# Kernel optimization log

Hardware: AMD Instinct MI355X
Metric: run time of the kernel (lower is better)

The kernel has to match this reference:

```python
import jax, jax.numpy as jnp
import numpy as np

N_NODES = 100000
N_EDGES = 3200000
IN_CH = 128
HID = 64
OUT_CH = 40


def setup_inputs() -> dict:
    key = jax.random.key(0)
    ks = jax.random.split(key, 12)
    x = jax.random.normal(ks[0], (N_NODES, IN_CH), dtype=jnp.float32)
    edge_index = jax.random.randint(ks[1], (2, N_EDGES), 0, N_NODES, dtype=jnp.int64)
    def lin(k, fan_in, fan_out):
        bound = 1.0 / np.sqrt(fan_in)
        kw, kb = jax.random.split(k)
        W = jax.random.uniform(kw, (fan_in, fan_out), minval=-bound, maxval=bound, dtype=jnp.float32)
        b = jax.random.uniform(kb, (fan_out,), minval=-bound, maxval=bound, dtype=jnp.float32)
        return W, b
    W1, b1 = lin(ks[2], IN_CH, HID)   # nn1 layer 1
    W2, b2 = lin(ks[3], HID, HID)     # nn1 layer 2
    W3, b3 = lin(ks[4], HID, HID)     # nn2 layer 1
    W4, b4 = lin(ks[5], HID, HID)     # nn2 layer 2
    Wf, bf = lin(ks[6], HID, OUT_CH)  # final fc
    return {"x": x, "edge_index": edge_index,
            "W1": W1, "b1": b1, "W2": W2, "b2": b2,
            "W3": W3, "b3": b3, "W4": W4, "b4": b4,
            "Wf": Wf, "bf": bf}


def _gin_conv(x, src, dst, W_a, b_a, W_b, b_b):
    # GINConv (eps=0): out = MLP(x + sum_{j->i} x_j)
    agg = jax.ops.segment_sum(x[src], dst, num_segments=x.shape[0])
    h = x + agg
    h = jax.nn.relu(h @ W_a + b_a)
    return h @ W_b + b_b


def reference(x, edge_index, W1, b1, W2, b2, W3, b3, W4, b4, Wf, bf):
    src, dst = edge_index[0], edge_index[1]
    h = _gin_conv(x, src, dst, W1, b1, W2, b2)
    h = jax.nn.relu(h)  # dropout is identity at eval
    h = _gin_conv(h, src, dst, W3, b3, W4, b4)
    h = jax.nn.relu(h)
    logits = h @ Wf + bf
    return jax.nn.log_softmax(logits, axis=1)
```

## Files before the change

kernel.cpp:

```cpp
#include <hip/hip_runtime.h>
#include <math.h>

#define N_NODES_C 100000
#define N_EDGES_C 3200000
#define NB 782
#define BNODES 128
#define LDS_CAP 6144
#define CHUNK 8192
#define NBLK 391

typedef unsigned short u16;
typedef __attribute__((ext_vector_type(8))) short short8v;
typedef __attribute__((ext_vector_type(4))) float float4v;

__device__ __forceinline__ float bf2f(u16 u) {
    unsigned int t = ((unsigned int)u) << 16;
    return __uint_as_float(t);
}
__device__ __forceinline__ u16 f2bf(float f) {
    unsigned int x = __float_as_uint(f);
    x += 0x7fffu + ((x >> 16) & 1u);
    return (u16)(x >> 16);
}


__global__ __launch_bounds__(256) void passA_hist_kernel(const int* __restrict__ dst,
                                                         int* __restrict__ cnt, int n_edges) {
    __shared__ int h[NB];
    for (int i = threadIdx.x; i < NB; i += 256) h[i] = 0;
    __syncthreads();
    const int blk = blockIdx.x;
    const int e0 = blk * CHUNK;
    const int cntE = min(CHUNK, n_edges - e0);
    for (int i = threadIdx.x * 4; i < cntE; i += 1024) {
        int4 d4 = *(const int4*)&dst[e0 + i];
        atomicAdd(&h[d4.x >> 7], 1); atomicAdd(&h[d4.y >> 7], 1);
        atomicAdd(&h[d4.z >> 7], 1); atomicAdd(&h[d4.w >> 7], 1);
    }
    __syncthreads();
    for (int i = threadIdx.x; i < NB; i += 256) cnt[i * NBLK + blk] = h[i];
}

__global__ __launch_bounds__(256) void scan_chunks_kernel(int* __restrict__ a, int n, int* __restrict__ bsums) {
    __shared__ int s[256];
    const int tid = threadIdx.x;
    int base = blockIdx.x * 1024 + tid * 4;
    int v[4];
#pragma unroll
    for (int i = 0; i < 4; ++i) v[i] = (base + i < n) ? a[base + i] : 0;
    int tsum = v[0] + v[1] + v[2] + v[3];
    s[tid] = tsum;
    __syncthreads();
    for (int off = 1; off < 256; off <<= 1) {
        int t = (tid >= off) ? s[tid - off] : 0;
        __syncthreads();
        s[tid] += t;
        __syncthreads();
    }
    int run = s[tid] - tsum;
#pragma unroll
    for (int i = 0; i < 4; ++i) {
        run += v[i];
        if (base + i < n) a[base + i] = run;
    }
    if (tid == 255) bsums[blockIdx.x] = s[255];
}

__global__ __launch_bounds__(512) void scan_sums_kernel(int* __restrict__ bsums, int nb) {
    __shared__ int s[512];
    const int tid = threadIdx.x;
    int v = (tid < nb) ? bsums[tid] : 0;
    s[tid] = v;
    __syncthreads();
    for (int off = 1; off < 512; off <<= 1) {
        int t = (tid >= off) ? s[tid - off] : 0;
        __syncthreads();
        s[tid] += t;
        __syncthreads();
    }
    if (tid < nb) bsums[tid] = s[tid] - v;
}

__global__ __launch_bounds__(256) void scan_add_kernel(int* __restrict__ a, int n, const int* __restrict__ bsums) {
    int base = blockIdx.x * 1024 + threadIdx.x * 4;
    int add = bsums[blockIdx.x];
#pragma unroll
    for (int i = 0; i < 4; ++i)
        if (base + i < n) a[base + i] += add;
}

__global__ __launch_bounds__(1024) void boffs_kernel(const int* __restrict__ incl,
                                                     int* __restrict__ boffs,
                                                     int* __restrict__ offs) {
    const int b = threadIdx.x;
    if (b < NB) boffs[b] = b ? incl[b * NBLK - 1] : 0;
    if (b == 0) {
        int total = incl[NB * NBLK - 1];
        boffs[NB] = total;
        offs[N_NODES_C] = total;
    }
}

__global__ __launch_bounds__(256) void passB_sort_kernel(const int* __restrict__ src,
                                                         const int* __restrict__ dst,
                                                         const int* __restrict__ incl,
                                                         unsigned int* __restrict__ stage,
                                                         int n_edges) {
    __shared__ unsigned int spack[CHUNK];
    __shared__ int hist[NB];
    __shared__ int lcur[NB];
    __shared__ int tsum[256];
    const int blk = blockIdx.x, tid = threadIdx.x;
    const int e0 = blk * CHUNK;
    const int cntE = min(CHUNK, n_edges - e0);

    for (int b = tid; b < NB; b += 256) hist[b] = 0;
    __syncthreads();

    for (int i = tid * 4; i < cntE; i += 1024) {
        int4 d4 = *(const int4*)&dst[e0 + i];
        atomicAdd(&hist[d4.x >> 7], 1); atomicAdd(&hist[d4.y >> 7], 1);
        atomicAdd(&hist[d4.z >> 7], 1); atomicAdd(&hist[d4.w >> 7], 1);
    }
    __syncthreads();

    {
        int loc[4];
        const int bi = tid * 4;
        int s = 0;
#pragma unroll
        for (int k = 0; k < 4; ++k) {
            int idx = bi + k;
            loc[k] = (idx < NB) ? hist[idx] : 0;
            s += loc[k];
        }
        tsum[tid] = s;
        __syncthreads();
        for (int off = 1; off < 256; off <<= 1) {
            int t = (tid >= off) ? tsum[tid - off] : 0;
            __syncthreads();
            tsum[tid] += t;
            __syncthreads();
        }
        int run = tsum[tid] - s;
#pragma unroll
        for (int k = 0; k < 4; ++k) {
            int idx = bi + k;
            if (idx < NB) {
                int h = loc[k];
                hist[idx] = run;
                lcur[idx] = run;
                run += h;
            }
        }
    }
    __syncthreads();

    for (int i = tid * 4; i < cntE; i += 1024) {
        int4 d4 = *(const int4*)&dst[e0 + i];
        int4 s4 = *(const int4*)&src[e0 + i];
        int p;
        p = atomicAdd(&lcur[d4.x >> 7], 1); spack[p] = (unsigned)s4.x | (((unsigned)d4.x & 127u) << 17);
        p = atomicAdd(&lcur[d4.y >> 7], 1); spack[p] = (unsigned)s4.y | (((unsigned)d4.y & 127u) << 17);
        p = atomicAdd(&lcur[d4.z >> 7], 1); spack[p] = (unsigned)s4.z | (((unsigned)d4.z & 127u) << 17);
        p = atomicAdd(&lcur[d4.w >> 7], 1); spack[p] = (unsigned)s4.w | (((unsigned)d4.w & 127u) << 17);
    }
    __syncthreads();

    for (int b = tid; b < NB; b += 256) {
        int l0 = hist[b];
        int l1 = (b + 1 < NB) ? hist[b + 1] : cntE;
        int idx = b * NBLK + blk;
        int g0 = idx ? incl[idx - 1] : 0;
        for (int j = l0; j < l1; ++j) stage[g0 + (j - l0)] = spack[j];
    }
}

__global__ __launch_bounds__(256) void bucket_finalize_kernel(const unsigned int* __restrict__ stage,
                                                              const int* __restrict__ boffs,
                                                              int* __restrict__ offs,
                                                              int* __restrict__ srcs) {
    __shared__ int hist[BNODES];
    __shared__ int excl[BNODES];
    __shared__ int curs[BNODES];
    __shared__ int sbuf[LDS_CAP];
    const int b = blockIdx.x, tid = threadIdx.x;
    const int base = boffs[b];
    const int count = boffs[b + 1] - base;
    const int n0 = b * BNODES;
    for (int i = tid; i < BNODES; i += 256) hist[i] = 0;
    __syncthreads();
    for (int i = tid; i < count; i += 256) {
        unsigned int w = stage[base + i];
        atomicAdd(&hist[w >> 17], 1);
    }
    __syncthreads();
    if (tid < BNODES) excl[tid] = hist[tid];
    __syncthreads();
    for (int off = 1; off < BNODES; off <<= 1) {
        int t = 0;
        if (tid < BNODES && tid >= off) t = excl[tid - off];
        __syncthreads();
        if (tid < BNODES) excl[tid] += t;
        __syncthreads();
    }
    if (tid < BNODES) {
        int ex = excl[tid] - hist[tid];
        int n = n0 + tid;
        if (n < N_NODES_C) offs[n] = base + ex;
        curs[tid] = ex;
    }
    __syncthreads();
    if (count <= LDS_CAP) {
        for (int i = tid; i < count; i += 256) {
            unsigned int w = stage[base + i];
            int p = atomicAdd(&curs[w >> 17], 1);
            sbuf[p] = (int)(w & 0x1FFFFu);
        }
        __syncthreads();
        for (int i = tid; i < count; i += 256) srcs[base + i] = sbuf[i];
    } else {
        for (int i = tid; i < count; i += 256) {
            unsigned int w = stage[base + i];
            int p = atomicAdd(&curs[w >> 17], 1);
            srcs[base + p] = (int)(w & 0x1FFFFu);
        }
    }
}


__global__ __launch_bounds__(256) void gather64v_kernel(const u16* __restrict__ feat,
                                                        const int* __restrict__ offs,
                                                        const int* __restrict__ srcs,
                                                        const float* __restrict__ bias,
                                                        u16* __restrict__ out, int n_nodes) {
    const int wave = threadIdx.x >> 6;
    const int lane = threadIdx.x & 63;
    const int grp  = lane >> 4;
    const int cl   = lane & 15;
    const int n = blockIdx.x * 4 + wave;
    if (n >= n_nodes) return;

    float a0 = 0.f, a1 = 0.f, a2 = 0.f, a3 = 0.f;
    if (grp == 0) {
        ushort4 v = *(const ushort4*)&feat[(size_t)n * 64 + cl * 4];
        a0 = bf2f(v.x); a1 = bf2f(v.y); a2 = bf2f(v.z); a3 = bf2f(v.w);
    }
    const int s0 = offs[n], s1 = offs[n + 1];
    int i = s0;
    for (; i + 32 <= s1; i += 32) {
        int r[8];
#pragma unroll
        for (int u = 0; u < 8; ++u) r[u] = srcs[i + u * 4 + grp];
        ushort4 v[8];
#pragma unroll
        for (int u = 0; u < 8; ++u) v[u] = *(const ushort4*)&feat[(size_t)r[u] * 64 + cl * 4];
#pragma unroll
        for (int u = 0; u < 8; ++u) {
            a0 += bf2f(v[u].x); a1 += bf2f(v[u].y); a2 += bf2f(v[u].z); a3 += bf2f(v[u].w);
        }
    }
    for (; i + 8 <= s1; i += 8) {
        int ra = srcs[i + grp];
        int rb = srcs[i + 4 + grp];
        ushort4 va = *(const ushort4*)&feat[(size_t)ra * 64 + cl * 4];
        ushort4 vb = *(const ushort4*)&feat[(size_t)rb * 64 + cl * 4];
        a0 += bf2f(va.x); a1 += bf2f(va.y); a2 += bf2f(va.z); a3 += bf2f(va.w);
        a0 += bf2f(vb.x); a1 += bf2f(vb.y); a2 += bf2f(vb.z); a3 += bf2f(vb.w);
    }
    for (; i + 4 <= s1; i += 4) {
        int rr = srcs[i + grp];
        ushort4 v = *(const ushort4*)&feat[(size_t)rr * 64 + cl * 4];
        a0 += bf2f(v.x); a1 += bf2f(v.y); a2 += bf2f(v.z); a3 += bf2f(v.w);
    }
    if (i + grp < s1) {
        int rr = srcs[i + grp];
        ushort4 v = *(const ushort4*)&feat[(size_t)rr * 64 + cl * 4];
        a0 += bf2f(v.x); a1 += bf2f(v.y); a2 += bf2f(v.z); a3 += bf2f(v.w);
    }
    a0 += __shfl_xor(a0, 16); a1 += __shfl_xor(a1, 16);
    a2 += __shfl_xor(a2, 16); a3 += __shfl_xor(a3, 16);
    a0 += __shfl_xor(a0, 32); a1 += __shfl_xor(a1, 32);
    a2 += __shfl_xor(a2, 32); a3 += __shfl_xor(a3, 32);
    if (lane < 16) {
        float4 b = *(const float4*)&bias[cl * 4];
        ushort4 o;
        o.x = f2bf(fmaxf(a0 + b.x, 0.f));
        o.y = f2bf(fmaxf(a1 + b.y, 0.f));
        o.z = f2bf(fmaxf(a2 + b.z, 0.f));
        o.w = f2bf(fmaxf(a3 + b.w, 0.f));
        *(ushort4*)&out[(size_t)n * 64 + cl * 4] = o;
    }
}

#define GIN_STEP(ai, i)                                                                               \
    acc[i][0] += ai.x * w0.x; acc[i][1] += ai.x * w0.y; acc[i][2] += ai.x * w0.z; acc[i][3] += ai.x * w0.w; \
    acc[i][0] += ai.y * w1.x; acc[i][1] += ai.y * w1.y; acc[i][2] += ai.y * w1.z; acc[i][3] += ai.y * w1.w; \
    acc[i][0] += ai.z * w2.x; acc[i][1] += ai.z * w2.y; acc[i][2] += ai.z * w2.z; acc[i][3] += ai.z * w2.w; \
    acc[i][0] += ai.w * w3.x; acc[i][1] += ai.w * w3.y; acc[i][2] += ai.w * w3.z; acc[i][3] += ai.w * w3.w;


__global__ __launch_bounds__(256) void dense128_kernel(const float* __restrict__ in,
                                                       const float* __restrict__ W,
                                                       u16* __restrict__ out, int n_nodes) {
    __shared__ float sW[128 * 64];
    const int tid = threadIdx.x;
    for (int i = tid; i < 128 * 16; i += 256) ((float4*)sW)[i] = ((const float4*)W)[i];
    __syncthreads();
    const int tj = tid & 15, tn = tid >> 4;
    const int j0 = tj * 4, n0 = blockIdx.x * 64 + tn * 4;
    const int r0 = min(n0 + 0, n_nodes - 1), r1 = min(n0 + 1, n_nodes - 1);
    const int r2 = min(n0 + 2, n_nodes - 1), r3 = min(n0 + 3, n_nodes - 1);
    float acc[4][4];
#pragma unroll
    for (int i = 0; i < 4; ++i)
#pragma unroll
        for (int j = 0; j < 4; ++j) acc[i][j] = 0.f;
#pragma unroll 4
    for (int k = 0; k < 128; k += 4) {
        float4 a0 = *(const float4*)&in[(size_t)r0 * 128 + k];
        float4 a1 = *(const float4*)&in[(size_t)r1 * 128 + k];
        float4 a2 = *(const float4*)&in[(size_t)r2 * 128 + k];
        float4 a3 = *(const float4*)&in[(size_t)r3 * 128 + k];
        float4 w0 = *(const float4*)&sW[(k + 0) * 64 + j0];
        float4 w1 = *(const float4*)&sW[(k + 1) * 64 + j0];
        float4 w2 = *(const float4*)&sW[(k + 2) * 64 + j0];
        float4 w3 = *(const float4*)&sW[(k + 3) * 64 + j0];
        GIN_STEP(a0, 0) GIN_STEP(a1, 1) GIN_STEP(a2, 2) GIN_STEP(a3, 3)
    }
#pragma unroll
    for (int i = 0; i < 4; ++i) {
        int n = n0 + i;
        if (n < n_nodes) {
            ushort4 o;
            o.x = f2bf(acc[i][0]); o.y = f2bf(acc[i][1]);
            o.z = f2bf(acc[i][2]); o.w = f2bf(acc[i][3]);
            *(ushort4*)&out[(size_t)n * 64 + j0] = o;
        }
    }
}


__global__ __launch_bounds__(256) void mfma_w2w3_kernel(const u16* __restrict__ in,
                                                        const float* __restrict__ W2,
                                                        const float* __restrict__ b2,
                                                        const float* __restrict__ W3,
                                                        u16* __restrict__ out, int n_nodes) {
    __shared__ u16 w2f[4096];
    __shared__ u16 w3f[4096];
    __shared__ u16 sT[64 * 72];
    const int tid = threadIdx.x;
    for (int idx = tid; idx < 4096; idx += 256) {
        int frag = idx >> 9;
        int within = idx & 511;
        int lane = within >> 3;
        int i = within & 7;
        int kt = frag >> 2, jt = frag & 3;
        int k = kt * 32 + (lane >> 4) * 8 + i;
        int j = jt * 16 + (lane & 15);
        w2f[idx] = f2bf(W2[k * 64 + j]);
        w3f[idx] = f2bf(W3[k * 64 + j]);
    }
    __syncthreads();
    const int w = tid >> 6, l = tid & 63;
    const int nbase = blockIdx.x * 64 + w * 16;
    const int arow = min(nbase + (l & 15), n_nodes - 1);
    short8v a0 = *(const short8v*)&in[(size_t)arow * 64 + (l >> 4) * 8];
    short8v a1 = *(const short8v*)&in[(size_t)arow * 64 + 32 + (l >> 4) * 8];
#pragma unroll
    for (int jt = 0; jt < 4; ++jt) {
        float bv = b2[jt * 16 + (l & 15)];
        float4v acc = {bv, bv, bv, bv};
        acc = __builtin_amdgcn_mfma_f32_16x16x32_bf16(a0, *(short8v*)&w2f[(0 * 4 + jt) * 512 + l * 8], acc, 0, 0, 0);
        acc = __builtin_amdgcn_mfma_f32_16x16x32_bf16(a1, *(short8v*)&w2f[(1 * 4 + jt) * 512 + l * 8], acc, 0, 0, 0);
#pragma unroll
        for (int r = 0; r < 4; ++r) {
            int row = w * 16 + (l >> 4) * 4 + r;
            sT[row * 72 + jt * 16 + (l & 15)] = f2bf(fmaxf(acc[r], 0.f));
        }
    }
    __syncthreads();
    const int trow = w * 16 + (l & 15);
    short8v t0 = *(short8v*)&sT[trow * 72 + (l >> 4) * 8];
    short8v t1 = *(short8v*)&sT[trow * 72 + 32 + (l >> 4) * 8];
#pragma unroll
    for (int jt = 0; jt < 4; ++jt) {
        float4v acc = {0.f, 0.f, 0.f, 0.f};
        acc = __builtin_amdgcn_mfma_f32_16x16x32_bf16(t0, *(short8v*)&w3f[(0 * 4 + jt) * 512 + l * 8], acc, 0, 0, 0);
        acc = __builtin_amdgcn_mfma_f32_16x16x32_bf16(t1, *(short8v*)&w3f[(1 * 4 + jt) * 512 + l * 8], acc, 0, 0, 0);
#pragma unroll
        for (int r = 0; r < 4; ++r) {
            int n = nbase + (l >> 4) * 4 + r;
            if (n < n_nodes) out[(size_t)n * 64 + jt * 16 + (l & 15)] = f2bf(acc[r]);
        }
    }
}


__global__ __launch_bounds__(256) void mfma_w4final_kernel(const u16* __restrict__ in,
                                                           const float* __restrict__ W4,
                                                           const float* __restrict__ b4,
                                                           const float* __restrict__ Wf,
                                                           const float* __restrict__ bfin,
                                                           float* __restrict__ out, int n_nodes) {
    __shared__ u16 w4f[4096];
    __shared__ u16 wff[3072];
    __shared__ u16 sT[64 * 72];
    __shared__ float sLog[64 * 40];
    const int tid = threadIdx.x;
    for (int idx = tid; idx < 4096; idx += 256) {
        int frag = idx >> 9;
        int within = idx & 511;
        int lane = within >> 3;
        int i = within & 7;
        int kt = frag >> 2, jt = frag & 3;
        int k = kt * 32 + (lane >> 4) * 8 + i;
        int j = jt * 16 + (lane & 15);
        w4f[idx] = f2bf(W4[k * 64 + j]);
    }
    for (int idx = tid; idx < 3072; idx += 256) {
        int frag = idx >> 9;
        int within = idx & 511;
        int lane = within >> 3;
        int i = within & 7;
        int kt = frag / 3, jt = frag % 3;
        int k = kt * 32 + (lane >> 4) * 8 + i;
        int j = jt * 16 + (lane & 15);
        wff[idx] = (j < 40) ? f2bf(Wf[k * 40 + j]) : (u16)0;
    }
    __syncthreads();
    const int w = tid >> 6, l = tid & 63;
    const int nbase = blockIdx.x * 64 + w * 16;
    const int arow = min(nbase + (l & 15), n_nodes - 1);
    short8v a0 = *(const short8v*)&in[(size_t)arow * 64 + (l >> 4) * 8];
    short8v a1 = *(const short8v*)&in[(size_t)arow * 64 + 32 + (l >> 4) * 8];
#pragma unroll
    for (int jt = 0; jt < 4; ++jt) {
        float bv = b4[jt * 16 + (l & 15)];
        float4v acc = {bv, bv, bv, bv};
        acc = __builtin_amdgcn_mfma_f32_16x16x32_bf16(a0, *(short8v*)&w4f[(0 * 4 + jt) * 512 + l * 8], acc, 0, 0, 0);
        acc = __builtin_amdgcn_mfma_f32_16x16x32_bf16(a1, *(short8v*)&w4f[(1 * 4 + jt) * 512 + l * 8], acc, 0, 0, 0);
#pragma unroll
        for (int r = 0; r < 4; ++r) {
            int row = w * 16 + (l >> 4) * 4 + r;
            sT[row * 72 + jt * 16 + (l & 15)] = f2bf(fmaxf(acc[r], 0.f));
        }
    }
    __syncthreads();
    const int trow = w * 16 + (l & 15);
    short8v t0 = *(short8v*)&sT[trow * 72 + (l >> 4) * 8];
    short8v t1 = *(short8v*)&sT[trow * 72 + 32 + (l >> 4) * 8];
#pragma unroll
    for (int jt = 0; jt < 3; ++jt) {
        int col = jt * 16 + (l & 15);
        float bv = (col < 40) ? bfin[col] : 0.f;
        float4v acc = {bv, bv, bv, bv};
        acc = __builtin_amdgcn_mfma_f32_16x16x32_bf16(t0, *(short8v*)&wff[(0 * 3 + jt) * 512 + l * 8], acc, 0, 0, 0);
        acc = __builtin_amdgcn_mfma_f32_16x16x32_bf16(t1, *(short8v*)&wff[(1 * 3 + jt) * 512 + l * 8], acc, 0, 0, 0);
#pragma unroll
        for (int r = 0; r < 4; ++r) {
            int row = w * 16 + (l >> 4) * 4 + r;
            if (col < 40) sLog[row * 40 + col] = acc[r];
        }
    }
    __syncthreads();
    if (tid < 64) {
        const int nl = tid;
        const int n = blockIdx.x * 64 + nl;
        if (n < n_nodes) {
            float m = -1e30f;
            for (int j = 0; j < 40; ++j) m = fmaxf(m, sLog[nl * 40 + j]);
            float s = 0.f;
            for (int j = 0; j < 40; ++j) s += expf(sLog[nl * 40 + j] - m);
            float lse = m + logf(s);
            for (int j = 0; j < 40; j += 4) {
                float4 o;
                o.x = sLog[nl * 40 + j + 0] - lse;
                o.y = sLog[nl * 40 + j + 1] - lse;
                o.z = sLog[nl * 40 + j + 2] - lse;
                o.w = sLog[nl * 40 + j + 3] - lse;
                *(float4*)&out[(size_t)n * 40 + j] = o;
            }
        }
    }
}


extern "C" void kernel_launch(void* const* d_in, const int* in_sizes, int n_in,
                              void* d_out, int out_size, void* d_ws, size_t ws_size,
                              hipStream_t stream) {
    const float* x  = (const float*)d_in[0];
    const int*   ei = (const int*)d_in[1];
    const float* W1 = (const float*)d_in[2];
    const float* b1 = (const float*)d_in[3];
    const float* W2 = (const float*)d_in[4];
    const float* b2 = (const float*)d_in[5];
    const float* W3 = (const float*)d_in[6];
    const float* b3 = (const float*)d_in[7];
    const float* W4 = (const float*)d_in[8];
    const float* b4 = (const float*)d_in[9];
    const float* Wf = (const float*)d_in[10];
    const float* bf = (const float*)d_in[11];
    float* outp = (float*)d_out;

    const int N = N_NODES_C, E = N_EDGES_C;
    const int* srcp = ei;
    const int* dstp = ei + E;

    char* ws = (char*)d_ws;
    int*          offs  = (int*)(ws);
    int*          boffs = (int*)(ws + 400128);
    int*          bsums = (int*)(ws + 403328);
    int*          cnt   = (int*)(ws + 405376);
    unsigned int* stage = (unsigned int*)(ws + 1628672);
    int*          srcs  = (int*)(ws + 14428672);
    u16*          Ybf   = (u16*)(ws + 27228672);
    u16*          F2bf  = (u16*)(ws + 40028672);

    passA_hist_kernel<<<NBLK, 256, 0, stream>>>(dstp, cnt, E);
    const int n_scan = NB * NBLK;
    const int nblk_scan = (n_scan + 1023) / 1024;
    scan_chunks_kernel<<<nblk_scan, 256, 0, stream>>>(cnt, n_scan, bsums);
    scan_sums_kernel<<<1, 512, 0, stream>>>(bsums, nblk_scan);
    scan_add_kernel<<<nblk_scan, 256, 0, stream>>>(cnt, n_scan, bsums);
    boffs_kernel<<<1, 1024, 0, stream>>>(cnt, boffs, offs);
    passB_sort_kernel<<<NBLK, 256, 0, stream>>>(srcp, dstp, cnt, stage, E);
    bucket_finalize_kernel<<<NB, 256, 0, stream>>>(stage, boffs, offs, srcs);

    const int mlp_grid = (N + 63) / 64;
    const int gat_grid = (N + 3) / 4;

    dense128_kernel<<<mlp_grid, 256, 0, stream>>>(x, W1, Ybf, N);
    gather64v_kernel<<<gat_grid, 256, 0, stream>>>(Ybf, offs, srcs, b1, F2bf, N);
    mfma_w2w3_kernel<<<mlp_grid, 256, 0, stream>>>(F2bf, W2, b2, W3, Ybf, N);

    gather64v_kernel<<<gat_grid, 256, 0, stream>>>(Ybf, offs, srcs, b3, F2bf, N);
    mfma_w4final_kernel<<<mlp_grid, 256, 0, stream>>>(F2bf, W4, b4, Wf, bf, outp, N);
}
```

Before: 263.7 us.

## Fuse CSR build into cooperative kernel and use MFMA for first dense layer

Merges the histogram, three-stage scan, bucket-offset computation and edge sort into a single cooperative kernel that uses grid-wide syncs, removing six kernel launches. The sort pass now recomputes the per-block histogram instead of keeping it across syncs. The first 128->64 dense layer is also rewritten to use bf16 MFMA instructions instead of scalar FP32 FMAs, which rounds the input x to bf16 and so reduces precision. Cooperative launch requires all 391 blocks to be co-resident and adds grid-barrier overhead.

```diff
diff --git a/kernel.cpp b/kernel.cpp
--- a/kernel.cpp
+++ b/kernel.cpp
@@ -1,5 +1,8 @@
 #include <hip/hip_runtime.h>
+#include <hip/hip_cooperative_groups.h>
 #include <math.h>
+
+namespace cg = cooperative_groups;
 
 #define N_NODES_C 100000
 #define N_EDGES_C 3200000
@@ -8,6 +11,8 @@
 #define LDS_CAP 6144
 #define CHUNK 8192
 #define NBLK 391
+#define NSCAN (NB * NBLK)
+#define NBLK_SCAN ((NSCAN + 1023) / 1024)
 
 typedef unsigned short u16;
 typedef __attribute__((ext_vector_type(8))) short short8v;
@@ -24,88 +29,15 @@
 }
 
 
-__global__ __launch_bounds__(256) void passA_hist_kernel(const int* __restrict__ dst,
-                                                         int* __restrict__ cnt, int n_edges) {
-    __shared__ int h[NB];
-    for (int i = threadIdx.x; i < NB; i += 256) h[i] = 0;
-    __syncthreads();
-    const int blk = blockIdx.x;
-    const int e0 = blk * CHUNK;
-    const int cntE = min(CHUNK, n_edges - e0);
-    for (int i = threadIdx.x * 4; i < cntE; i += 1024) {
-        int4 d4 = *(const int4*)&dst[e0 + i];
-        atomicAdd(&h[d4.x >> 7], 1); atomicAdd(&h[d4.y >> 7], 1);
-        atomicAdd(&h[d4.z >> 7], 1); atomicAdd(&h[d4.w >> 7], 1);
-    }
-    __syncthreads();
-    for (int i = threadIdx.x; i < NB; i += 256) cnt[i * NBLK + blk] = h[i];
-}
-
-__global__ __launch_bounds__(256) void scan_chunks_kernel(int* __restrict__ a, int n, int* __restrict__ bsums) {
-    __shared__ int s[256];
-    const int tid = threadIdx.x;
-    int base = blockIdx.x * 1024 + tid * 4;
-    int v[4];
-#pragma unroll
-    for (int i = 0; i < 4; ++i) v[i] = (base + i < n) ? a[base + i] : 0;
-    int tsum = v[0] + v[1] + v[2] + v[3];
-    s[tid] = tsum;
-    __syncthreads();
-    for (int off = 1; off < 256; off <<= 1) {
-        int t = (tid >= off) ? s[tid - off] : 0;
-        __syncthreads();
-        s[tid] += t;
-        __syncthreads();
-    }
-    int run = s[tid] - tsum;
-#pragma unroll
-    for (int i = 0; i < 4; ++i) {
-        run += v[i];
-        if (base + i < n) a[base + i] = run;
-    }
-    if (tid == 255) bsums[blockIdx.x] = s[255];
-}
-
-__global__ __launch_bounds__(512) void scan_sums_kernel(int* __restrict__ bsums, int nb) {
-    __shared__ int s[512];
-    const int tid = threadIdx.x;
-    int v = (tid < nb) ? bsums[tid] : 0;
-    s[tid] = v;
-    __syncthreads();
-    for (int off = 1; off < 512; off <<= 1) {
-        int t = (tid >= off) ? s[tid - off] : 0;
-        __syncthreads();
-        s[tid] += t;
-        __syncthreads();
-    }
-    if (tid < nb) bsums[tid] = s[tid] - v;
-}
-
-__global__ __launch_bounds__(256) void scan_add_kernel(int* __restrict__ a, int n, const int* __restrict__ bsums) {
-    int base = blockIdx.x * 1024 + threadIdx.x * 4;
-    int add = bsums[blockIdx.x];
-#pragma unroll
-    for (int i = 0; i < 4; ++i)
-        if (base + i < n) a[base + i] += add;
-}
-
-__global__ __launch_bounds__(1024) void boffs_kernel(const int* __restrict__ incl,
-                                                     int* __restrict__ boffs,
-                                                     int* __restrict__ offs) {
-    const int b = threadIdx.x;
-    if (b < NB) boffs[b] = b ? incl[b * NBLK - 1] : 0;
-    if (b == 0) {
-        int total = incl[NB * NBLK - 1];
-        boffs[NB] = total;
-        offs[N_NODES_C] = total;
-    }
-}
-
-__global__ __launch_bounds__(256) void passB_sort_kernel(const int* __restrict__ src,
-                                                         const int* __restrict__ dst,
-                                                         const int* __restrict__ incl,
-                                                         unsigned int* __restrict__ stage,
-                                                         int n_edges) {
+__global__ __launch_bounds__(256) void csr_coop_kernel(const int* __restrict__ src,
+                                                       const int* __restrict__ dst,
+                                                       int* __restrict__ cnt,
+                                                       int* __restrict__ bsums,
+                                                       int* __restrict__ boffs,
+                                                       int* __restrict__ offs,
+                                                       unsigned int* __restrict__ stage,
+                                                       int n_edges) {
+    cg::grid_group grid = cg::this_grid();
     __shared__ unsigned int spack[CHUNK];
     __shared__ int hist[NB];
     __shared__ int lcur[NB];
@@ -116,14 +48,86 @@
 
     for (int b = tid; b < NB; b += 256) hist[b] = 0;
     __syncthreads();
-
     for (int i = tid * 4; i < cntE; i += 1024) {
         int4 d4 = *(const int4*)&dst[e0 + i];
         atomicAdd(&hist[d4.x >> 7], 1); atomicAdd(&hist[d4.y >> 7], 1);
         atomicAdd(&hist[d4.z >> 7], 1); atomicAdd(&hist[d4.w >> 7], 1);
     }
     __syncthreads();
-
+    for (int i = tid; i < NB; i += 256) cnt[i * NBLK + blk] = hist[i];
+    grid.sync();
+
+    if (blk < NBLK_SCAN) {
+        int base = blk * 1024 + tid * 4;
+        int v[4];
+#pragma unroll
+        for (int i = 0; i < 4; ++i) v[i] = (base + i < NSCAN) ? cnt[base + i] : 0;
+        int ts = v[0] + v[1] + v[2] + v[3];
+        tsum[tid] = ts;
+        __syncthreads();
+        for (int off = 1; off < 256; off <<= 1) {
+            int t = (tid >= off) ? tsum[tid - off] : 0;
+            __syncthreads();
+            tsum[tid] += t;
+            __syncthreads();
+        }
+        int run = tsum[tid] - ts;
+#pragma unroll
+        for (int i = 0; i < 4; ++i) {
+            run += v[i];
+            if (base + i < NSCAN) cnt[base + i] = run;
+        }
+        if (tid == 255) bsums[blk] = tsum[255];
+    }
+    grid.sync();
+
+    if (blk == 0) {
+        int i0 = tid * 2, i1 = tid * 2 + 1;
+        int e0v = (i0 < NBLK_SCAN) ? bsums[i0] : 0;
+        int e1v = (i1 < NBLK_SCAN) ? bsums[i1] : 0;
+        int ps = e0v + e1v;
+        tsum[tid] = ps;
+        __syncthreads();
+        for (int off = 1; off < 256; off <<= 1) {
+            int t = (tid >= off) ? tsum[tid - off] : 0;
+            __syncthreads();
+            tsum[tid] += t;
+            __syncthreads();
+        }
+        int ex = tsum[tid] - ps;
+        if (i0 < NBLK_SCAN) bsums[i0] = ex;
+        if (i1 < NBLK_SCAN) bsums[i1] = ex + e0v;
+    }
+    grid.sync();
+
+    if (blk < NBLK_SCAN) {
+        int base = blk * 1024 + tid * 4;
+        int add = bsums[blk];
+#pragma unroll
+        for (int i = 0; i < 4; ++i) {
+            int idx = base + i;
+            if (idx < NSCAN) {
+                int v = cnt[idx] + add;
+                cnt[idx] = v;
+                if (((idx + 1) % NBLK) == 0) {
+                    int b = (idx + 1) / NBLK;
+                    boffs[b] = v;
+                    if (b == NB) offs[N_NODES_C] = v;
+                }
+            }
+        }
+        if (blk == 0 && tid == 0) boffs[0] = 0;
+    }
+    grid.sync();
+
+    for (int b = tid; b < NB; b += 256) hist[b] = 0;
+    __syncthreads();
+    for (int i = tid * 4; i < cntE; i += 1024) {
+        int4 d4 = *(const int4*)&dst[e0 + i];
+        atomicAdd(&hist[d4.x >> 7], 1); atomicAdd(&hist[d4.y >> 7], 1);
+        atomicAdd(&hist[d4.z >> 7], 1); atomicAdd(&hist[d4.w >> 7], 1);
+    }
+    __syncthreads();
     {
         int loc[4];
         const int bi = tid * 4;
@@ -155,7 +159,6 @@
         }
     }
     __syncthreads();
-
     for (int i = tid * 4; i < cntE; i += 1024) {
         int4 d4 = *(const int4*)&dst[e0 + i];
         int4 s4 = *(const int4*)&src[e0 + i];
@@ -166,12 +169,11 @@
         p = atomicAdd(&lcur[d4.w >> 7], 1); spack[p] = (unsigned)s4.w | (((unsigned)d4.w & 127u) << 17);
     }
     __syncthreads();
-
     for (int b = tid; b < NB; b += 256) {
         int l0 = hist[b];
         int l1 = (b + 1 < NB) ? hist[b + 1] : cntE;
         int idx = b * NBLK + blk;
-        int g0 = idx ? incl[idx - 1] : 0;
+        int g0 = idx ? cnt[idx - 1] : 0;
         for (int j = l0; j < l1; ++j) stage[g0 + (j - l0)] = spack[j];
     }
 }
@@ -293,49 +295,48 @@
     }
 }
 
-#define GIN_STEP(ai, i)                                                                               \
-    acc[i][0] += ai.x * w0.x; acc[i][1] += ai.x * w0.y; acc[i][2] += ai.x * w0.z; acc[i][3] += ai.x * w0.w; \
-    acc[i][0] += ai.y * w1.x; acc[i][1] += ai.y * w1.y; acc[i][2] += ai.y * w1.z; acc[i][3] += ai.y * w1.w; \
-    acc[i][0] += ai.z * w2.x; acc[i][1] += ai.z * w2.y; acc[i][2] += ai.z * w2.z; acc[i][3] += ai.z * w2.w; \
-    acc[i][0] += ai.w * w3.x; acc[i][1] += ai.w * w3.y; acc[i][2] += ai.w * w3.z; acc[i][3] += ai.w * w3.w;
-
-
-__global__ __launch_bounds__(256) void dense128_kernel(const float* __restrict__ in,
-                                                       const float* __restrict__ W,
-                                                       u16* __restrict__ out, int n_nodes) {
-    __shared__ float sW[128 * 64];
+
+__global__ __launch_bounds__(256) void mfma_dense128_kernel(const float* __restrict__ in,
+                                                            const float* __restrict__ W,
+                                                            u16* __restrict__ out, int n_nodes) {
+    __shared__ u16 w1f[16 * 512];
     const int tid = threadIdx.x;
-    for (int i = tid; i < 128 * 16; i += 256) ((float4*)sW)[i] = ((const float4*)W)[i];
-    __syncthreads();
-    const int tj = tid & 15, tn = tid >> 4;
-    const int j0 = tj * 4, n0 = blockIdx.x * 64 + tn * 4;
-    const int r0 = min(n0 + 0, n_nodes - 1), r1 = min(n0 + 1, n_nodes - 1);
-    const int r2 = min(n0 + 2, n_nodes - 1), r3 = min(n0 + 3, n_nodes - 1);
-    float acc[4][4];
-#pragma unroll
-    for (int i = 0; i < 4; ++i)
-#pragma unroll
-        for (int j = 0; j < 4; ++j) acc[i][j] = 0.f;
-#pragma unroll 4
-    for (int k = 0; k < 128; k += 4) {
-        float4 a0 = *(const float4*)&in[(size_t)r0 * 128 + k];
-        float4 a1 = *(const float4*)&in[(size_t)r1 * 128 + k];
-        float4 a2 = *(const float4*)&in[(size_t)r2 * 128 + k];
-        float4 a3 = *(const float4*)&in[(size_t)r3 * 128 + k];
-        float4 w0 = *(const float4*)&sW[(k + 0) * 64 + j0];
-        float4 w1 = *(const float4*)&sW[(k + 1) * 64 + j0];
-        float4 w2 = *(const float4*)&sW[(k + 2) * 64 + j0];
-        float4 w3 = *(const float4*)&sW[(k + 3) * 64 + j0];
-        GIN_STEP(a0, 0) GIN_STEP(a1, 1) GIN_STEP(a2, 2) GIN_STEP(a3, 3)
-    }
-#pragma unroll
-    for (int i = 0; i < 4; ++i) {
-        int n = n0 + i;
-        if (n < n_nodes) {
-            ushort4 o;
-            o.x = f2bf(acc[i][0]); o.y = f2bf(acc[i][1]);
-            o.z = f2bf(acc[i][2]); o.w = f2bf(acc[i][3]);
-            *(ushort4*)&out[(size_t)n * 64 + j0] = o;
+    for (int idx = tid; idx < 8192; idx += 256) {
+        int frag = idx >> 9;
+        int within = idx & 511;
+        int lane = within >> 3;
+        int i = within & 7;
+        int kt = frag >> 2, jt = frag & 3;
+        int k = kt * 32 + (lane >> 4) * 8 + i;
+        int j = jt * 16 + (lane & 15);
+        w1f[idx] = f2bf(W[k * 64 + j]);
+    }
+    __syncthreads();
+    const int w = tid >> 6, l = tid & 63;
+    const int nbase = blockIdx.x * 64 + w * 16;
+    const int arow = min(nbase + (l & 15), n_nodes - 1);
+    short8v a[4];
+#pragma unroll
+    for (int kt = 0; kt < 4; ++kt) {
+        float4 f0 = *(const float4*)&in[(size_t)arow * 128 + kt * 32 + (l >> 4) * 8];
+        float4 f1 = *(const float4*)&in[(size_t)arow * 128 + kt * 32 + (l >> 4) * 8 + 4];
+        short8v t;
+        t[0] = (short)f2bf(f0.x); t[1] = (short)f2bf(f0.y);
+        t[2] = (short)f2bf(f0.z); t[3] = (short)f2bf(f0.w);
+        t[4] = (short)f2bf(f1.x); t[5] = (short)f2bf(f1.y);
+        t[6] = (short)f2bf(f1.z); t[7] = (short)f2bf(f1.w);
+        a[kt] = t;
+    }
+#pragma unroll
+    for (int jt = 0; jt < 4; ++jt) {
+        float4v acc = {0.f, 0.f, 0.f, 0.f};
+#pragma unroll
+        for (int kt = 0; kt < 4; ++kt)
+            acc = __builtin_amdgcn_mfma_f32_16x16x32_bf16(a[kt], *(short8v*)&w1f[(kt * 4 + jt) * 512 + l * 8], acc, 0, 0, 0);
+#pragma unroll
+        for (int r = 0; r < 4; ++r) {
+            int n = nbase + (l >> 4) * 4 + r;
+            if (n < n_nodes) out[(size_t)n * 64 + jt * 16 + (l & 15)] = f2bf(acc[r]);
         }
     }
 }
@@ -517,20 +518,18 @@
     u16*          Ybf   = (u16*)(ws + 27228672);
     u16*          F2bf  = (u16*)(ws + 40028672);
 
-    passA_hist_kernel<<<NBLK, 256, 0, stream>>>(dstp, cnt, E);
-    const int n_scan = NB * NBLK;
-    const int nblk_scan = (n_scan + 1023) / 1024;
-    scan_chunks_kernel<<<nblk_scan, 256, 0, stream>>>(cnt, n_scan, bsums);
-    scan_sums_kernel<<<1, 512, 0, stream>>>(bsums, nblk_scan);
-    scan_add_kernel<<<nblk_scan, 256, 0, stream>>>(cnt, n_scan, bsums);
-    boffs_kernel<<<1, 1024, 0, stream>>>(cnt, boffs, offs);
-    passB_sort_kernel<<<NBLK, 256, 0, stream>>>(srcp, dstp, cnt, stage, E);
+    {
+        int E_val = E;
+        void* args[] = {(void*)&srcp, (void*)&dstp, (void*)&cnt, (void*)&bsums,
+                        (void*)&boffs, (void*)&offs, (void*)&stage, (void*)&E_val};
+        hipLaunchCooperativeKernel((void*)csr_coop_kernel, dim3(NBLK), dim3(256), args, 0, stream);
+    }
     bucket_finalize_kernel<<<NB, 256, 0, stream>>>(stage, boffs, offs, srcs);
 
     const int mlp_grid = (N + 63) / 64;
     const int gat_grid = (N + 3) / 4;
 
-    dense128_kernel<<<mlp_grid, 256, 0, stream>>>(x, W1, Ybf, N);
+    mfma_dense128_kernel<<<mlp_grid, 256, 0, stream>>>(x, W1, Ybf, N);
     gather64v_kernel<<<gat_grid, 256, 0, stream>>>(Ybf, offs, srcs, b1, F2bf, N);
     mfma_w2w3_kernel<<<mlp_grid, 256, 0, stream>>>(F2bf, W2, b2, W3, Ybf, N);
 
```

Measured after the change: 449.4 us. 70.5% more time.
